# Kernel tuning notes

Hardware: AMD Instinct MI355X
Metric: run time of the kernel (lower is better)

## Reference

```python
import jax, jax.numpy as jnp
import numpy as np

N_JOINTS = 50
N_BONES = 50
# getSkeletalModelStructure() stand-in: 50 bones over 50 joints (i -> (i+1) % 50)
SRC = jnp.arange(N_BONES)
DST = (jnp.arange(N_BONES) + 1) % N_JOINTS
EPS = 1e-8


def _length_direct(x):
    # x: [B, T, 150] -> lengths [B, T, 50], directions [B, T, 150]
    B, T, _ = x.shape
    joints = x.reshape(B, T, N_JOINTS, 3)
    diff = joints[:, :, SRC, :] - joints[:, :, DST, :]      # [B, T, 50, 3]
    length = jnp.sqrt(jnp.sum(diff * diff, axis=-1))        # [B, T, 50]
    direct = diff / (length[..., None] + EPS)               # [B, T, 50, 3]
    return length, direct.reshape(B, T, N_BONES * 3)


def setup_inputs() -> dict:
    key = jax.random.key(0)
    k1, k2 = jax.random.split(key)
    preds = jax.random.normal(k1, (128, 1024, 150), dtype=jnp.float32)
    targets = jax.random.normal(k2, (128, 1024, 150), dtype=jnp.float32)
    return {"preds": preds, "targets": targets}


def reference(preds, targets):
    target_pad = 0.0
    loss_mask = (targets != target_pad).astype(jnp.float32)
    preds_masked = preds * loss_mask
    targets_masked = targets * loss_mask
    _, pd = _length_direct(preds_masked)
    _, td = _length_direct(targets_masked)
    pd = pd * loss_mask[:, :, :150]
    td = td * loss_mask[:, :, :150]
    # criterion = L1 (mean), criterion_bone = MSE (mean); loss_scale = 1.0
    loss = jnp.mean(jnp.abs(preds_masked - targets_masked)) + 0.1 * jnp.mean((pd - td) ** 2)
    return loss
```

## Files before the change

kernel.cpp:

```cpp
#include <hip/hip_runtime.h>


#define ROW_F    150
#define ROWS_PB  32
#define SPAN_F   (ROWS_PB * ROW_F)
#define SPAN_F4  (SPAN_F / 4)
#define GRID     1024

__global__ __launch_bounds__(256, 4) void loss_kernel(
    const float* __restrict__ preds,
    const float* __restrict__ targets,
    float* __restrict__ out,
    int iters, float inv_count)
{
    const float EPS = 1e-8f;
    __shared__ float sp[SPAN_F];
    __shared__ float st[SPAN_F];
    __shared__ float wsum[4];

    const int tid  = threadIdx.x;
    const int lane = tid & 63;
    const int wid  = tid >> 6;

    const float4* gp4 = reinterpret_cast<const float4*>(preds);
    const float4* gt4 = reinterpret_cast<const float4*>(targets);
    float4* sp4 = reinterpret_cast<float4*>(sp);
    float4* st4 = reinterpret_cast<float4*>(st);

    const int g0 = tid, g1 = tid + 256, g2 = tid + 512, g3 = tid + 768, g4 = tid + 1024;
    const bool w4 = (g4 < SPAN_F4);
    const int g4c = w4 ? g4 : (SPAN_F4 - 1);

    const int seg = tid >> 5;
    const int row = tid & 31;
    const int j0 = (seg < 2) ? seg * 7 : 14 + (seg - 2) * 6;
    const int j1 = (seg < 2) ? j0 + 7  : j0 + 6;

    float l1 = 0.0f, mse = 0.0f;

    size_t sb = (size_t)blockIdx.x * SPAN_F4;
    float4 rp0 = gp4[sb + g0], rp1 = gp4[sb + g1], rp2 = gp4[sb + g2],
           rp3 = gp4[sb + g3], rp4 = gp4[sb + g4c];
    float4 rt0 = gt4[sb + g0], rt1 = gt4[sb + g1], rt2 = gt4[sb + g2],
           rt3 = gt4[sb + g3], rt4 = gt4[sb + g4c];

    for (int it = 0; it < iters; ++it) {
        if (it) __syncthreads();

        sp4[g0] = rp0; st4[g0] = rt0;
        sp4[g1] = rp1; st4[g1] = rt1;
        sp4[g2] = rp2; st4[g2] = rt2;
        sp4[g3] = rp3; st4[g3] = rt3;
        if (w4) { sp4[g4] = rp4; st4[g4] = rt4; }
        __syncthreads();

        if (it + 1 < iters) {
            size_t nb = (size_t)(blockIdx.x + (size_t)(it + 1) * GRID) * SPAN_F4;
            rp0 = gp4[nb + g0]; rp1 = gp4[nb + g1]; rp2 = gp4[nb + g2];
            rp3 = gp4[nb + g3]; rp4 = gp4[nb + g4c];
            rt0 = gt4[nb + g0]; rt1 = gt4[nb + g1]; rt2 = gt4[nb + g2];
            rt3 = gt4[nb + g3]; rt4 = gt4[nb + g4c];
        }

        const float* rpb = sp + row * ROW_F;
        const float* rtb = st + row * ROW_F;

        float pmP[3], tmP[3];
#pragma unroll
        for (int c = 0; c < 3; ++c) {
            float t = rtb[3 * j0 + c];
            float p = rpb[3 * j0 + c];
            pmP[c] = (t != 0.0f) ? p : 0.0f;
            tmP[c] = t;
            l1 += fabsf(pmP[c] - tmP[c]);
        }

        for (int b = j0; b < j1; ++b) {
            int jn = b + 1;
            if (jn == 50) jn = 0;
            float pmN[3], tmN[3];
#pragma unroll
            for (int c = 0; c < 3; ++c) {
                float t = rtb[3 * jn + c];
                float p = rpb[3 * jn + c];
                pmN[c] = (t != 0.0f) ? p : 0.0f;
                tmN[c] = t;
            }
            if (jn < j1 && jn != 0) {
#pragma unroll
                for (int c = 0; c < 3; ++c) l1 += fabsf(pmN[c] - tmN[c]);
            }
            float dp[3], dt[3], lp = 0.0f, lt = 0.0f;
#pragma unroll
            for (int c = 0; c < 3; ++c) {
                dp[c] = pmP[c] - pmN[c];
                dt[c] = tmP[c] - tmN[c];
                lp += dp[c] * dp[c];
                lt += dt[c] * dt[c];
            }
            float ip = __builtin_amdgcn_rcpf(__builtin_amdgcn_sqrtf(lp) + EPS);
            float iq = __builtin_amdgcn_rcpf(__builtin_amdgcn_sqrtf(lt) + EPS);
#pragma unroll
            for (int c = 0; c < 3; ++c) {
                float d = dp[c] * ip - dt[c] * iq;
                d = (tmP[c] != 0.0f) ? d : 0.0f;
                mse += d * d;
            }
#pragma unroll
            for (int c = 0; c < 3; ++c) { pmP[c] = pmN[c]; tmP[c] = tmN[c]; }
        }
    }

    float part = (l1 + 0.1f * mse) * inv_count;
#pragma unroll
    for (int off = 32; off > 0; off >>= 1)
        part += __shfl_down(part, off, 64);

    if (lane == 0) wsum[wid] = part;
    __syncthreads();
    if (tid == 0) {
        float s = wsum[0] + wsum[1] + wsum[2] + wsum[3];
        atomicAdd(out, s);
    }
}

extern "C" void kernel_launch(void* const* d_in, const int* in_sizes, int n_in,
                              void* d_out, int out_size, void* d_ws, size_t ws_size,
                              hipStream_t stream)
{
    const float* preds   = (const float*)d_in[0];
    const float* targets = (const float*)d_in[1];
    float* out = (float*)d_out;

    hipMemsetAsync(out, 0, sizeof(float) * out_size, stream);

    int n_elems = in_sizes[0];
    int n_rows  = n_elems / ROW_F;
    int spans   = n_rows / ROWS_PB;
    float inv_count = 1.0f / (float)n_elems;

    int iters = spans / GRID;
    loss_kernel<<<GRID, 256, 0, stream>>>(preds, targets, out, iters, inv_count);
}
```

Measured before the change: 173.8 us.

## Give each wave a private LDS span and drop block barriers

Each wave now stages and processes its own 8-row span in a private slice of shared memory, so the per-iteration __syncthreads barriers are removed. The thread mapping changes to 8 lanes per row with 8 bone segments. The L1 term is computed directly from the float4 registers loaded from global memory instead of inside the bone loop. This removes block-wide synchronisation stalls and shortens the bone loop. It relies on wave-level ordering of LDS writes and reads with no explicit wave barrier, and it changes the LDS bank access pattern.

```diff
diff --git a/kernel.cpp b/kernel.cpp
--- a/kernel.cpp
+++ b/kernel.cpp
@@ -2,10 +2,12 @@
 
 
 #define ROW_F    150
-#define ROWS_PB  32
-#define SPAN_F   (ROWS_PB * ROW_F)
+#define ROWS_PW  8
+#define SPAN_F   (ROWS_PW * ROW_F)
 #define SPAN_F4  (SPAN_F / 4)
+#define WAVES_PB 4
 #define GRID     1024
+#define TOTAL_WAVES (GRID * WAVES_PB)
 
 __global__ __launch_bounds__(256, 4) void loss_kernel(
     const float* __restrict__ preds,
@@ -14,9 +16,9 @@
     int iters, float inv_count)
 {
     const float EPS = 1e-8f;
-    __shared__ float sp[SPAN_F];
-    __shared__ float st[SPAN_F];
-    __shared__ float wsum[4];
+    __shared__ float sp[WAVES_PB][SPAN_F];
+    __shared__ float st[WAVES_PB][SPAN_F];
+    __shared__ float wsum[WAVES_PB];
 
     const int tid  = threadIdx.x;
     const int lane = tid & 63;
@@ -24,46 +26,55 @@
 
     const float4* gp4 = reinterpret_cast<const float4*>(preds);
     const float4* gt4 = reinterpret_cast<const float4*>(targets);
-    float4* sp4 = reinterpret_cast<float4*>(sp);
-    float4* st4 = reinterpret_cast<float4*>(st);
+    float4* sp4 = reinterpret_cast<float4*>(sp[wid]);
+    float4* st4 = reinterpret_cast<float4*>(st[wid]);
 
-    const int g0 = tid, g1 = tid + 256, g2 = tid + 512, g3 = tid + 768, g4 = tid + 1024;
+    const int g0 = lane, g1 = lane + 64, g2 = lane + 128, g3 = lane + 192, g4 = lane + 256;
     const bool w4 = (g4 < SPAN_F4);
     const int g4c = w4 ? g4 : (SPAN_F4 - 1);
 
-    const int seg = tid >> 5;
-    const int row = tid & 31;
+    const int row = lane >> 3;
+    const int seg = lane & 7;
     const int j0 = (seg < 2) ? seg * 7 : 14 + (seg - 2) * 6;
-    const int j1 = (seg < 2) ? j0 + 7  : j0 + 6;
+    const int j1 = (seg < 2) ? j0 + 7 : j0 + 6;
 
     float l1 = 0.0f, mse = 0.0f;
 
-    size_t sb = (size_t)blockIdx.x * SPAN_F4;
+    const int wglobal = blockIdx.x * WAVES_PB + wid;
+
+    size_t sb = (size_t)wglobal * SPAN_F4;
     float4 rp0 = gp4[sb + g0], rp1 = gp4[sb + g1], rp2 = gp4[sb + g2],
            rp3 = gp4[sb + g3], rp4 = gp4[sb + g4c];
     float4 rt0 = gt4[sb + g0], rt1 = gt4[sb + g1], rt2 = gt4[sb + g2],
            rt3 = gt4[sb + g3], rt4 = gt4[sb + g4c];
 
+#define L1ACC(P, T) do {                                         \
+        l1 += ((T).x != 0.0f) ? fabsf((P).x - (T).x) : 0.0f;     \
+        l1 += ((T).y != 0.0f) ? fabsf((P).y - (T).y) : 0.0f;     \
+        l1 += ((T).z != 0.0f) ? fabsf((P).z - (T).z) : 0.0f;     \
+        l1 += ((T).w != 0.0f) ? fabsf((P).w - (T).w) : 0.0f;     \
+    } while (0)
+
     for (int it = 0; it < iters; ++it) {
-        if (it) __syncthreads();
-
         sp4[g0] = rp0; st4[g0] = rt0;
         sp4[g1] = rp1; st4[g1] = rt1;
         sp4[g2] = rp2; st4[g2] = rt2;
         sp4[g3] = rp3; st4[g3] = rt3;
         if (w4) { sp4[g4] = rp4; st4[g4] = rt4; }
-        __syncthreads();
+
+        L1ACC(rp0, rt0); L1ACC(rp1, rt1); L1ACC(rp2, rt2); L1ACC(rp3, rt3);
+        if (w4) L1ACC(rp4, rt4);
 
         if (it + 1 < iters) {
-            size_t nb = (size_t)(blockIdx.x + (size_t)(it + 1) * GRID) * SPAN_F4;
+            size_t nb = (size_t)(wglobal + (size_t)(it + 1) * TOTAL_WAVES) * SPAN_F4;
             rp0 = gp4[nb + g0]; rp1 = gp4[nb + g1]; rp2 = gp4[nb + g2];
             rp3 = gp4[nb + g3]; rp4 = gp4[nb + g4c];
             rt0 = gt4[nb + g0]; rt1 = gt4[nb + g1]; rt2 = gt4[nb + g2];
             rt3 = gt4[nb + g3]; rt4 = gt4[nb + g4c];
         }
 
-        const float* rpb = sp + row * ROW_F;
-        const float* rtb = st + row * ROW_F;
+        const float* rpb = &sp[wid][row * ROW_F];
+        const float* rtb = &st[wid][row * ROW_F];
 
         float pmP[3], tmP[3];
 #pragma unroll
@@ -72,7 +83,6 @@
             float p = rpb[3 * j0 + c];
             pmP[c] = (t != 0.0f) ? p : 0.0f;
             tmP[c] = t;
-            l1 += fabsf(pmP[c] - tmP[c]);
         }
 
         for (int b = j0; b < j1; ++b) {
@@ -85,10 +95,6 @@
                 float p = rpb[3 * jn + c];
                 pmN[c] = (t != 0.0f) ? p : 0.0f;
                 tmN[c] = t;
-            }
-            if (jn < j1 && jn != 0) {
-#pragma unroll
-                for (int c = 0; c < 3; ++c) l1 += fabsf(pmN[c] - tmN[c]);
             }
             float dp[3], dt[3], lp = 0.0f, lt = 0.0f;
 #pragma unroll
@@ -119,8 +125,7 @@
     if (lane == 0) wsum[wid] = part;
     __syncthreads();
     if (tid == 0) {
-        float s = wsum[0] + wsum[1] + wsum[2] + wsum[3];
-        atomicAdd(out, s);
+        atomicAdd(out, wsum[0] + wsum[1] + wsum[2] + wsum[3]);
     }
 }
 
@@ -136,9 +141,9 @@
 
     int n_elems = in_sizes[0];
     int n_rows  = n_elems / ROW_F;
-    int spans   = n_rows / ROWS_PB;
+    int spans   = n_rows / ROWS_PW;
     float inv_count = 1.0f / (float)n_elems;
 
-    int iters = spans / GRID;
+    int iters = spans / TOTAL_WAVES;
     loss_kernel<<<GRID, 256, 0, stream>>>(preds, targets, out, iters, inv_count);
 }
```

After: 174.0 us. No clear change (+0.1%).
